# Kernel optimization log

Hardware: AMD Instinct MI355X
Metric: run time of the kernel (lower is better)

The kernel has to match this reference:

```python
import jax, jax.numpy as jnp
import numpy as np
import math

L, D, H, DK, DFF, B, S = 4, 512, 8, 256, 2048, 8, 256
HD = H * DK
EPS = 1e-6


def _norm(x, alpha, bias):
    # torch: alpha*(x-mean)/(std_unbiased + eps) + bias  (std uses ddof=1)
    mu = x.mean(axis=-1, keepdims=True)
    var = ((x - mu) ** 2).sum(axis=-1, keepdims=True) / (x.shape[-1] - 1)
    return alpha * (x - mu) / (jnp.sqrt(var) + EPS) + bias


def _positional_encoding():
    pos = jnp.arange(S, dtype=jnp.float32)[:, None]          # [S,1]
    i = jnp.arange(0, D, 2, dtype=jnp.float32)               # even indices
    pe_sin = jnp.sin(pos / (S ** (2.0 * i / D)))             # [S,D/2]
    pe_cos = jnp.cos(pos / (S ** (2.0 * (i + 1.0) / D)))     # [S,D/2]
    pe = jnp.zeros((S, D), dtype=jnp.float32)
    pe = pe.at[:, 0::2].set(pe_sin).at[:, 1::2].set(pe_cos)
    return pe


def setup_inputs() -> dict:
    key = jax.random.key(0)
    ks = jax.random.split(key, 16)
    sc = 0.02
    inp = {
        "data": jax.random.normal(ks[0], (B, S, D), dtype=jnp.float32),
        "attn_m": jax.random.randint(ks[1], (B, S), 0, 2, dtype=jnp.int32),
        "view_idx": 0,
        "seg_emb": jax.random.normal(ks[2], (3, D), dtype=jnp.float32) * sc,
        "Wq": jax.random.normal(ks[3], (L, D, HD), dtype=jnp.float32) * sc,
        "bq": jnp.zeros((L, HD), dtype=jnp.float32),
        "Wk": jax.random.normal(ks[4], (L, D, HD), dtype=jnp.float32) * sc,
        "bk": jnp.zeros((L, HD), dtype=jnp.float32),
        "Wv": jax.random.normal(ks[5], (L, D, HD), dtype=jnp.float32) * sc,
        "bv": jnp.zeros((L, HD), dtype=jnp.float32),
        "Wo": jax.random.normal(ks[6], (L, HD, D), dtype=jnp.float32) * sc,
        "bo": jnp.zeros((L, D), dtype=jnp.float32),
        "W1": jax.random.normal(ks[7], (L, D, DFF), dtype=jnp.float32) * sc,
        "b1": jnp.zeros((L, DFF), dtype=jnp.float32),
        "W2": jax.random.normal(ks[8], (L, DFF, D), dtype=jnp.float32) * sc,
        "b2": jnp.zeros((L, D), dtype=jnp.float32),
        "alpha1": jnp.ones((L, D), dtype=jnp.float32),
        "bias1": jnp.zeros((L, D), dtype=jnp.float32),
        "alpha2": jnp.ones((L, D), dtype=jnp.float32),
        "bias2": jnp.zeros((L, D), dtype=jnp.float32),
        "alpha_f": jnp.ones((D,), dtype=jnp.float32),
        "bias_f": jnp.zeros((D,), dtype=jnp.float32),
    }
    return inp


def reference(data, attn_m, view_idx, seg_emb, Wq, bq, Wk, bk, Wv, bv, Wo, bo,
              W1, b1, W2, b2, alpha1, bias1, alpha2, bias2, alpha_f, bias_f):
    # positional encoder: x*sqrt(d_f) + pe + seg_embedding(view_idx*seq_len)
    pe = _positional_encoding()
    seg_idx = view_idx * S  # scalar; must be < 3 (view_idx == 0 in practice)
    x = data * math.sqrt(D) + pe[None, :, :] + seg_emb[seg_idx][None, None, :]

    # mask: attn_m [B,S] -> [B,1,1,S] bool, True = masked (key axis)
    maskb = attn_m.astype(bool)[:, None, None, :]

    for i in range(L):
        x2 = _norm(x, alpha1[i], bias1[i])
        q = (x2 @ Wq[i] + bq[i]).reshape(B, S, H, DK).transpose(0, 2, 1, 3)
        k = (x2 @ Wk[i] + bk[i]).reshape(B, S, H, DK).transpose(0, 2, 1, 3)
        v = (x2 @ Wv[i] + bv[i]).reshape(B, S, H, DK).transpose(0, 2, 1, 3)
        scores = jnp.einsum('bhqd,bhkd->bhqk', q, k) / math.sqrt(DK)
        scores = jnp.where(maskb, -1e9, scores)
        attnw = jax.nn.softmax(scores, axis=-1)
        o = jnp.einsum('bhqk,bhkd->bhqd', attnw, v)
        o = o.transpose(0, 2, 1, 3).reshape(B, S, HD) @ Wo[i] + bo[i]
        x = x + o
        x2 = _norm(x, alpha2[i], bias2[i])
        ff = jax.nn.relu(x2 @ W1[i] + b1[i]) @ W2[i] + b2[i]
        x = x + ff

    return _norm(x, alpha_f, bias_f)
```

## Files before the change

### kernel.cpp

```cpp
#include <hip/hip_runtime.h>
#include <hip/hip_bf16.h>

#define LNUM 4
#define DIM  512
#define SS   256

typedef unsigned short ushort_t;
typedef __attribute__((ext_vector_type(8))) short bf16x8;
typedef __attribute__((ext_vector_type(4))) float f32x4;
typedef __attribute__((ext_vector_type(8))) unsigned short u16x8;

#define VWAIT(n) asm volatile("s_waitcnt vmcnt(" #n ")" ::: "memory")
__device__ __forceinline__ void bar() { __builtin_amdgcn_s_barrier(); }

__device__ __forceinline__ ushort_t f2b(float f) {
  union { float f; unsigned u; } x; x.f = f;
  unsigned r = x.u + 0x7FFFu + ((x.u >> 16) & 1u);
  return (ushort_t)(r >> 16);
}

__device__ __forceinline__ void gload16(const void* g, void* s) {
  __builtin_amdgcn_global_load_lds((const __attribute__((address_space(1))) void*)g,
                                   (__attribute__((address_space(3))) void*)s, 16, 0, 0);
}

template<int TM, int TN, int EPI, int NBUF>
__global__ __launch_bounds__(256, 2)
void gemm_bt(const ushort_t* __restrict__ A, const ushort_t* __restrict__ B,
             const float* __restrict__ bias, const float* __restrict__ bias2,
             const float* __restrict__ bias3,
             ushort_t* __restrict__ outB, ushort_t* __restrict__ outB2,
             ushort_t* __restrict__ outB3, float* __restrict__ outF,
             int K, int lda, int ldb, int ldc, int nkz, int relu,
             long zA, long zB)
{
  constexpr int CA = TM / 32, CB = TN / 32, SN = CA + CB;
  constexpr int WM = TM / 32, WN = TN / 32;
  constexpr bool BATCH = (EPI == 4);
  __shared__ ushort_t As[NBUF * TM * 64];
  __shared__ ushort_t Bs[NBUF * TN * 64];
  const int tid = threadIdx.x, lane = tid & 63, wid = tid >> 6;
  const int wm = wid >> 1, wn = wid & 1;
  const int z = blockIdx.z;
  const int kz = BATCH ? 0 : z;
  const int Kz = K / nkz, k0 = kz * Kz, nt = Kz >> 6;

  const ushort_t* Ab = A + (BATCH ? (long)z * zA : 0) + (long)blockIdx.y * TM * lda + k0;
  const ushort_t* Bb = B + (BATCH ? (long)z * zB : 0) + (long)blockIdx.x * TN * ldb + k0;

  const ushort_t* srcA[CA]; ushort_t* ldsA[CA];
  const ushort_t* srcB[CB]; ushort_t* ldsB[CB];
#pragma unroll
  for (int c = 0; c < CA; ++c) {
    int off = c * 4096 + tid * 16;
    int row = off >> 7;
    int scol = ((off & 127) ^ ((row & 7) << 4)) >> 1;
    srcA[c] = Ab + (long)row * lda + scol;
    ldsA[c] = As + c * 2048 + wid * 512;
  }
#pragma unroll
  for (int c = 0; c < CB; ++c) {
    int off = c * 4096 + tid * 16;
    int row = off >> 7;
    int scol = ((off & 127) ^ ((row & 7) << 4)) >> 1;
    srcB[c] = Bb + (long)row * ldb + scol;
    ldsB[c] = Bs + c * 2048 + wid * 512;
  }

  f32x4 acc[WM][WN] = {};

  auto STAGE = [&](int buf, int t) {
#pragma unroll
    for (int c = 0; c < CA; ++c) gload16(srcA[c] + t * 64, ldsA[c] + buf * TM * 64);
#pragma unroll
    for (int c = 0; c < CB; ++c) gload16(srcB[c] + t * 64, ldsB[c] + buf * TN * 64);
  };

  auto COMPUTE = [&](int buf) {
#pragma unroll
    for (int ks = 0; ks < 2; ++ks) {
      const int kb = ks * 64 + ((lane >> 4) << 4);
      bf16x8 af[WM], bfr[WN];
#pragma unroll
      for (int f = 0; f < WM; ++f) {
        int ra = wm * (TM / 2) + f * 16 + (lane & 15);
        af[f] = *(const bf16x8*)((const char*)As + buf * TM * 128 + ra * 128 + (kb ^ ((ra & 7) << 4)));
      }
#pragma unroll
      for (int g = 0; g < WN; ++g) {
        int rb = wn * (TN / 2) + g * 16 + (lane & 15);
        bfr[g] = *(const bf16x8*)((const char*)Bs + buf * TN * 128 + rb * 128 + (kb ^ ((rb & 7) << 4)));
      }
      __builtin_amdgcn_s_setprio(1);
#pragma unroll
      for (int i = 0; i < WM; ++i)
#pragma unroll
        for (int j = 0; j < WN; ++j)
          acc[i][j] = __builtin_amdgcn_mfma_f32_16x16x32_bf16(af[i], bfr[j], acc[i][j], 0, 0, 0);
      __builtin_amdgcn_s_setprio(0);
    }
  };

  STAGE(0, 0);
  if constexpr (NBUF == 3) {
    STAGE(1, 1);
    for (int t = 0; t < nt; ++t) {
      if (t < nt - 1) { if constexpr (SN == 6) VWAIT(6); else VWAIT(4); }
      else VWAIT(0);
      bar();
      if (t + 2 < nt) STAGE((t + 2) % 3, t + 2);
      COMPUTE(t % 3);
    }
  } else {
    for (int t = 0; t < nt; ++t) {
      VWAIT(0);
      bar();
      if (t + 1 < nt) STAGE((t + 1) & 1, t + 1);
      COMPUTE(t & 1);
    }
  }

  const int row0 = blockIdx.y * TM + wm * (TM / 2) + ((lane >> 4) << 2);
  int col0 = blockIdx.x * TN + wn * (TN / 2) + (lane & 15);
  const float* bsel = bias;
  ushort_t* osel = outB;
  int seg = 0;
  if (EPI == 3) {
    seg = (blockIdx.x * TN) >> 11;
    if (seg == 1) { bsel = bias2; osel = outB2; }
    else if (seg == 2) { bsel = bias3; }
    col0 -= seg * 2048;
  }

  if (EPI == 3 && seg == 2) {
    ushort_t* Vt = As;
    const int colvBase = blockIdx.x * TN - 4096;
    const int rowBase = blockIdx.y * TM;
    const int h = colvBase >> 8, dk0 = colvBase & 255;
    const int bh = ((rowBase >> 8) << 3) + h;
    const int s0 = rowBase & 255;
    bar();
    if constexpr (TN == 64) {
#pragma unroll
      for (int i = 0; i < WM; ++i)
#pragma unroll
        for (int j = 0; j < WN; ++j) {
          const int colL = wn * (TN / 2) + j * 16 + (lane & 15);
          const float bv = bsel[col0 + j * 16];
#pragma unroll
          for (int r = 0; r < 4; ++r) {
            const int rowL = wm * (TM / 2) + i * 16 + ((lane >> 4) << 2) + r;
            Vt[colL * 136 + rowL] = f2b(acc[i][j][r] + bv);
          }
        }
      bar();
      const int dkl = tid >> 2, scc = (tid & 3) * 32;
      ushort_t* dst = outB3 + ((long)bh << 16) + (long)(dk0 + dkl) * 256 + s0 + scc;
#pragma unroll
      for (int m = 0; m < 4; ++m)
        *(u16x8*)(dst + m * 8) = *(const u16x8*)(Vt + dkl * 136 + scc + m * 8);
    } else {
#pragma unroll
      for (int half = 0; half < 2; ++half) {
        if (half) bar();
        if (wn == half) {
#pragma unroll
          for (int i = 0; i < WM; ++i)
#pragma unroll
            for (int j = 0; j < WN; ++j) {
              const int colL = j * 16 + (lane & 15);
              const float bv = bsel[col0 + j * 16];
#pragma unroll
              for (int r = 0; r < 4; ++r) {
                const int rowL = wm * 64 + i * 16 + ((lane >> 4) << 2) + r;
                Vt[colL * 136 + rowL] = f2b(acc[i][j][r] + bv);
              }
            }
        }
        bar();
        const int dkl = tid >> 2, scc = (tid & 3) * 32;
        ushort_t* dst = outB3 + ((long)bh << 16) +
                        (long)(dk0 + half * 64 + dkl) * 256 + s0 + scc;
#pragma unroll
        for (int m = 0; m < 4; ++m)
          *(u16x8*)(dst + m * 8) = *(const u16x8*)(Vt + dkl * 136 + scc + m * 8);
      }
    }
    return;
  }

#pragma unroll
  for (int i = 0; i < WM; ++i) {
#pragma unroll
    for (int j = 0; j < WN; ++j) {
      const int col = col0 + j * 16;
      float bv = 0.f;
      if (EPI == 2) bv = (kz == 0) ? bias[col] : 0.f;
      else if (EPI == 0 || EPI == 3) bv = bsel[col];
#pragma unroll
      for (int r = 0; r < 4; ++r) {
        const int row = row0 + i * 16 + r;
        float v = acc[i][j][r] + bv;
        if (EPI == 2) {
          outF[(long)kz * 1048576 + (long)row * ldc + col] = v;
        } else if (EPI == 3) {
          const long addr = (((long)(row >> 8) * 8 + (col >> 8)) << 16) +
                            (long)(row & 255) * 256 + (col & 255);
          osel[addr] = f2b(v);
        } else if (EPI == 4) {
          const int bb = z >> 3, hh = z & 7;
          osel[(long)(bb * 256 + row) * 2048 + hh * 256 + col] = f2b(acc[i][j][r]);
        } else {
          if (relu) v = fmaxf(v, 0.f);
          osel[(long)row * ldc + col] = f2b(v);
        }
      }
    }
  }
}

__global__ __launch_bounds__(256, 2)
void scoresm_k(const ushort_t* __restrict__ qh, const ushort_t* __restrict__ kh,
               const int* __restrict__ attnm, ushort_t* __restrict__ P)
{
  __shared__ ushort_t As[2][64 * 64];
  __shared__ ushort_t Bs[2][256 * 64];
  const int bh = blockIdx.x, qt = blockIdx.y;
  const int b = bh >> 3;
  const int tid = threadIdx.x, lane = tid & 63, wid = tid >> 6;
  const int l15 = lane & 15, l4 = lane >> 4;

  unsigned mbits = 0;
#pragma unroll
  for (int j = 0; j < 16; ++j)
    mbits |= (attnm[b * 256 + j * 16 + l15] != 0 ? 1u : 0u) << j;

  const ushort_t* Qb = qh + ((long)bh << 16) + qt * 64 * 256;
  const ushort_t* Kb = kh + ((long)bh << 16);
  const ushort_t* srcA[2]; ushort_t* ldsA[2];
  const ushort_t* srcB[8]; ushort_t* ldsB[8];
#pragma unroll
  for (int c = 0; c < 2; ++c) {
    int off = c * 4096 + tid * 16;
    int row = off >> 7;
    int scol = ((off & 127) ^ ((row & 7) << 4)) >> 1;
    srcA[c] = Qb + (long)row * 256 + scol;
    ldsA[c] = As[0] + c * 2048 + wid * 512;
  }
#pragma unroll
  for (int c = 0; c < 8; ++c) {
    int off = c * 4096 + tid * 16;
    int row = off >> 7;
    int scol = ((off & 127) ^ ((row & 7) << 4)) >> 1;
    srcB[c] = Kb + (long)row * 256 + scol;
    ldsB[c] = Bs[0] + c * 2048 + wid * 512;
  }

  auto STAGE = [&](int buf, int t) {
#pragma unroll
    for (int c = 0; c < 2; ++c) gload16(srcA[c] + t * 64, ldsA[c] + buf * 4096);
#pragma unroll
    for (int c = 0; c < 8; ++c) gload16(srcB[c] + t * 64, ldsB[c] + buf * 16384);
  };

  f32x4 sacc[16] = {};
  STAGE(0, 0);
  for (int t = 0; t < 4; ++t) {
    VWAIT(0);
    bar();
    if (t < 3) STAGE((t + 1) & 1, t + 1);
    const int buf = t & 1;
#pragma unroll
    for (int ks = 0; ks < 2; ++ks) {
      const int kb = ks * 64 + (l4 << 4);
      const int ra = wid * 16 + l15;
      bf16x8 af = *(const bf16x8*)((const char*)As[buf] + ra * 128 + (kb ^ ((ra & 7) << 4)));
      __builtin_amdgcn_s_setprio(1);
#pragma unroll
      for (int j = 0; j < 16; ++j) {
        const int rb = j * 16 + l15;
        bf16x8 bf_ = *(const bf16x8*)((const char*)Bs[buf] + rb * 128 + (kb ^ ((rb & 7) << 4)));
        sacc[j] = __builtin_amdgcn_mfma_f32_16x16x32_bf16(af, bf_, sacc[j], 0, 0, 0);
      }
      __builtin_amdgcn_s_setprio(0);
    }
  }

  float mr[4] = {-3e38f, -3e38f, -3e38f, -3e38f}, sr[4] = {};
#pragma unroll
  for (int j = 0; j < 16; ++j) {
    const bool mk = (mbits >> j) & 1;
#pragma unroll
    for (int r = 0; r < 4; ++r) {
      float s = mk ? -1e9f : sacc[j][r] * 0.0625f;
      sacc[j][r] = s;
      mr[r] = fmaxf(mr[r], s);
    }
  }
#pragma unroll
  for (int o = 1; o < 16; o <<= 1)
#pragma unroll
    for (int r = 0; r < 4; ++r) mr[r] = fmaxf(mr[r], __shfl_xor(mr[r], o, 16));
#pragma unroll
  for (int j = 0; j < 16; ++j)
#pragma unroll
    for (int r = 0; r < 4; ++r) {
      float e = __expf(sacc[j][r] - mr[r]);
      sacc[j][r] = e;
      sr[r] += e;
    }
#pragma unroll
  for (int o = 1; o < 16; o <<= 1)
#pragma unroll
    for (int r = 0; r < 4; ++r) sr[r] += __shfl_xor(sr[r], o, 16);
#pragma unroll
  for (int r = 0; r < 4; ++r) sr[r] = 1.f / sr[r];

  ushort_t* Rp = (ushort_t*)Bs;
  bar();
#pragma unroll
  for (int j = 0; j < 16; ++j)
#pragma unroll
    for (int r = 0; r < 4; ++r) {
      const int row = wid * 16 + l4 * 4 + r;
      *(ushort_t*)((char*)Rp + row * 512 + (((j * 16 + l15) * 2) ^ ((row & 7) << 4))) =
          f2b(sacc[j][r] * sr[r]);
    }
  bar();
  const int row = tid >> 2, cb0 = (tid & 3) * 128;
  ushort_t* dst = P + ((long)bh << 16) + (long)(qt * 64 + row) * 256 + (cb0 >> 1);
#pragma unroll
  for (int m = 0; m < 8; ++m) {
    u16x8 v = *(const u16x8*)((const char*)Rp + row * 512 + ((cb0 + m * 16) ^ ((row & 7) << 4)));
    *(u16x8*)(dst + m * 8) = v;
  }
}

__global__ __launch_bounds__(256)
void build_x(const float* __restrict__ data, const float* __restrict__ seg,
             const int* __restrict__ viewp, float* __restrict__ x)
{
  int i = blockIdx.x * 256 + threadIdx.x;
  int d = i & 511;
  int s = (i >> 9) & 255;
  float ang = (float)s * exp2f((float)d * -0.03125f);
  float pe = (d & 1) ? cosf(ang) : sinf(ang);
  int vrow = viewp[0] * SS;
  x[i] = data[i] * 22.627416997969522f + pe + seg[vrow * DIM + d];
}

__global__ __launch_bounds__(256)
void lnorm_k(const float* __restrict__ x, const float* __restrict__ parts, int np,
             float* __restrict__ xout,
             const float* __restrict__ alpha, const float* __restrict__ beta,
             ushort_t* __restrict__ outB, float* __restrict__ outF)
{
  const int row = blockIdx.x, tid = threadIdx.x;
  const long base = (long)row * DIM;
  float2 v = ((const float2*)(x + base))[tid];
  if (np) {
    for (int p = 0; p < np; ++p) {
      float2 a = ((const float2*)(parts + (long)p * 1048576 + base))[tid];
      v.x += a.x; v.y += a.y;
    }
    ((float2*)(xout + base))[tid] = v;
  }
  float s = v.x + v.y;
#pragma unroll
  for (int o = 32; o; o >>= 1) s += __shfl_xor(s, o, 64);
  __shared__ float rs[4], rq[4];
  if ((tid & 63) == 0) rs[tid >> 6] = s;
  __syncthreads();
  const float mu = (rs[0] + rs[1] + rs[2] + rs[3]) * (1.f / 512.f);
  const float dx = v.x - mu, dy = v.y - mu;
  float q = dx * dx + dy * dy;
#pragma unroll
  for (int o = 32; o; o >>= 1) q += __shfl_xor(q, o, 64);
  if ((tid & 63) == 0) rq[tid >> 6] = q;
  __syncthreads();
  const float var = (rq[0] + rq[1] + rq[2] + rq[3]) * (1.f / 511.f);
  const float rstd = 1.f / (sqrtf(var) + 1e-6f);
  const int d0 = tid * 2;
  const float o0 = alpha[d0] * dx * rstd + beta[d0];
  const float o1 = alpha[d0 + 1] * dy * rstd + beta[d0 + 1];
  if (outB) { outB[base + d0] = f2b(o0); outB[base + d0 + 1] = f2b(o1); }
  else      { outF[base + d0] = o0;      outF[base + d0 + 1] = o1; }
}

__global__ __launch_bounds__(256)
void wtransA(const float* __restrict__ Wq, const float* __restrict__ Wk,
             const float* __restrict__ Wv, const float* __restrict__ W1,
             ushort_t* __restrict__ qkvW, ushort_t* __restrict__ W1T)
{
  __shared__ float t[32][33];
  const int z = blockIdx.z, widx = z >> 2, layer = z & 3;
  const float* src = (widx == 0) ? Wq : (widx == 1) ? Wk : (widx == 2) ? Wv : W1;
  src += (long)layer * 512 * 2048;
  ushort_t* dst = (widx == 3) ? (W1T + (long)layer * 2048 * 512)
                              : (qkvW + (long)layer * (6144L * 512) + (long)widx * 2048 * 512);
  const int c0 = blockIdx.x * 32, r0 = blockIdx.y * 32;
  const int tx = threadIdx.x & 31, ty = threadIdx.x >> 5;
#pragma unroll
  for (int i = 0; i < 4; ++i) t[ty + i * 8][tx] = src[(long)(r0 + ty + i * 8) * 2048 + c0 + tx];
  __syncthreads();
#pragma unroll
  for (int i = 0; i < 4; ++i) dst[(long)(c0 + ty + i * 8) * 512 + r0 + tx] = f2b(t[tx][ty + i * 8]);
}

__global__ __launch_bounds__(256)
void wtransB(const float* __restrict__ Wo, const float* __restrict__ W2,
             ushort_t* __restrict__ WoT, ushort_t* __restrict__ W2T)
{
  __shared__ float t[32][33];
  const int z = blockIdx.z, widx = z >> 2, layer = z & 3;
  const float* src = ((widx == 0) ? Wo : W2) + (long)layer * 2048 * 512;
  ushort_t* dst = ((widx == 0) ? WoT : W2T) + (long)layer * 512 * 2048;
  const int c0 = blockIdx.x * 32, r0 = blockIdx.y * 32;
  const int tx = threadIdx.x & 31, ty = threadIdx.x >> 5;
#pragma unroll
  for (int i = 0; i < 4; ++i) t[ty + i * 8][tx] = src[(long)(r0 + ty + i * 8) * 512 + c0 + tx];
  __syncthreads();
#pragma unroll
  for (int i = 0; i < 4; ++i) dst[(long)(c0 + ty + i * 8) * 2048 + r0 + tx] = f2b(t[tx][ty + i * 8]);
}

extern "C" void kernel_launch(void* const* d_in, const int* in_sizes, int n_in,
                              void* d_out, int out_size, void* d_ws, size_t ws_size,
                              hipStream_t stream)
{
  const float* data  = (const float*)d_in[0];
  const int*   attnm = (const int*)d_in[1];
  const int*   viewp = (const int*)d_in[2];
  const float* seg   = (const float*)d_in[3];
  const float* Wq    = (const float*)d_in[4];
  const float* bq    = (const float*)d_in[5];
  const float* Wk    = (const float*)d_in[6];
  const float* bk    = (const float*)d_in[7];
  const float* Wv    = (const float*)d_in[8];
  const float* bv    = (const float*)d_in[9];
  const float* Wo    = (const float*)d_in[10];
  const float* bo    = (const float*)d_in[11];
  const float* W1    = (const float*)d_in[12];
  const float* b1    = (const float*)d_in[13];
  const float* W2    = (const float*)d_in[14];
  const float* b2    = (const float*)d_in[15];
  const float* al1   = (const float*)d_in[16];
  const float* be1   = (const float*)d_in[17];
  const float* al2   = (const float*)d_in[18];
  const float* be2   = (const float*)d_in[19];
  const float* alf   = (const float*)d_in[20];
  const float* bef   = (const float*)d_in[21];

  char* w = (char*)d_ws;
  const size_t MB = 1024 * 1024;
  ushort_t* qkvW = (ushort_t*)(w + 0 * MB);
  ushort_t* WoT  = (ushort_t*)(w + 24 * MB);
  ushort_t* W1T  = (ushort_t*)(w + 32 * MB);
  ushort_t* W2T  = (ushort_t*)(w + 40 * MB);
  float*    x    = (float*)   (w + 48 * MB);
  ushort_t* x2   = (ushort_t*)(w + 52 * MB);
  ushort_t* qb   = (ushort_t*)(w + 54 * MB);
  ushort_t* kbf  = (ushort_t*)(w + 62 * MB);
  ushort_t* vT   = (ushort_t*)(w + 70 * MB);
  ushort_t* ao   = (ushort_t*)(w + 78 * MB);
  ushort_t* ffh  = (ushort_t*)(w + 86 * MB);
  float*    parts= (float*)   (w + 94 * MB);
  ushort_t* P    = (ushort_t*)(w + 110 * MB);

  dim3 blk(256);
  const long QKV_L = 6144L * 512;
  wtransA<<<dim3(64, 16, 16), blk, 0, stream>>>(Wq, Wk, Wv, W1, qkvW, W1T);
  wtransB<<<dim3(16, 64, 8), blk, 0, stream>>>(Wo, W2, WoT, W2T);
  build_x<<<4096, blk, 0, stream>>>(data, seg, viewp, x);

  for (int i = 0; i < LNUM; ++i) {
    if (i == 0)
      lnorm_k<<<2048, blk, 0, stream>>>(x, nullptr, 0, nullptr, al1, be1, x2, nullptr);
    gemm_bt<128, 128, 3, 2><<<dim3(48, 16, 1), blk, 0, stream>>>(
        x2, qkvW + (long)i * QKV_L, bq + i * 2048, bk + i * 2048, bv + i * 2048,
        qb, kbf, vT, nullptr, 512, 512, 512, 2048, 1, 0, 0, 0);
    scoresm_k<<<dim3(64, 4), blk, 0, stream>>>(qb, kbf, attnm, P);
    gemm_bt<128, 64, 4, 3><<<dim3(4, 2, 64), blk, 0, stream>>>(
        P, vT, nullptr, nullptr, nullptr,
        ao, nullptr, nullptr, nullptr, 256, 256, 256, 2048, 1, 0,
        65536, 65536);
    gemm_bt<64, 64, 2, 3><<<dim3(8, 32, 2), blk, 0, stream>>>(
        ao, WoT + (long)i * 512 * 2048, bo + i * 512, nullptr, nullptr,
        nullptr, nullptr, nullptr, parts, 2048, 2048, 2048, 512, 2, 0, 0, 0);
    lnorm_k<<<2048, blk, 0, stream>>>(x, parts, 2, x, al2 + i * 512, be2 + i * 512, x2, nullptr);
    gemm_bt<128, 64, 0, 3><<<dim3(32, 16, 1), blk, 0, stream>>>(
        x2, W1T + (long)i * 2048 * 512, b1 + i * 2048, nullptr, nullptr,
        ffh, nullptr, nullptr, nullptr, 512, 512, 512, 2048, 1, 1, 0, 0);
    gemm_bt<64, 64, 2, 3><<<dim3(8, 32, 2), blk, 0, stream>>>(
        ffh, W2T + (long)i * 512 * 2048, b2 + i * 512, nullptr, nullptr,
        nullptr, nullptr, nullptr, parts, 2048, 2048, 2048, 512, 2, 0, 0, 0);
    if (i < LNUM - 1)
      lnorm_k<<<2048, blk, 0, stream>>>(x, parts, 2, x, al1 + (i + 1) * 512, be1 + (i + 1) * 512, x2, nullptr);
    else
      lnorm_k<<<2048, blk, 0, stream>>>(x, parts, 2, x, alf, bef, nullptr, (float*)d_out);
  }
}
```

Baseline: 431.4 us.

## Fuse attention P·V product into the scores/softmax kernel

The softmax kernel now keeps the normalized probability tile in LDS and loads it into registers. It then streams V^T chunks through double-buffered LDS to compute P·V with MFMA, writing the head output directly into the concatenated layout. This removes the separate batched GEMM launch and the global round trip of the probability matrix P. In exchange, the attention work runs on only 256 blocks with more serial work each, which may leave much of the GPU idle.

```diff
diff --git a/kernel.cpp b/kernel.cpp
--- a/kernel.cpp
+++ b/kernel.cpp
@@ -31,22 +31,19 @@
              const float* __restrict__ bias3,
              ushort_t* __restrict__ outB, ushort_t* __restrict__ outB2,
              ushort_t* __restrict__ outB3, float* __restrict__ outF,
-             int K, int lda, int ldb, int ldc, int nkz, int relu,
-             long zA, long zB)
+             int K, int lda, int ldb, int ldc, int nkz, int relu)
 {
   constexpr int CA = TM / 32, CB = TN / 32, SN = CA + CB;
   constexpr int WM = TM / 32, WN = TN / 32;
-  constexpr bool BATCH = (EPI == 4);
   __shared__ ushort_t As[NBUF * TM * 64];
   __shared__ ushort_t Bs[NBUF * TN * 64];
   const int tid = threadIdx.x, lane = tid & 63, wid = tid >> 6;
   const int wm = wid >> 1, wn = wid & 1;
-  const int z = blockIdx.z;
-  const int kz = BATCH ? 0 : z;
+  const int kz = blockIdx.z;
   const int Kz = K / nkz, k0 = kz * Kz, nt = Kz >> 6;
 
-  const ushort_t* Ab = A + (BATCH ? (long)z * zA : 0) + (long)blockIdx.y * TM * lda + k0;
-  const ushort_t* Bb = B + (BATCH ? (long)z * zB : 0) + (long)blockIdx.x * TN * ldb + k0;
+  const ushort_t* Ab = A + (long)blockIdx.y * TM * lda + k0;
+  const ushort_t* Bb = B + (long)blockIdx.x * TN * ldb + k0;
 
   const ushort_t* srcA[CA]; ushort_t* ldsA[CA];
   const ushort_t* srcB[CB]; ushort_t* ldsB[CB];
@@ -140,51 +137,30 @@
     const int bh = ((rowBase >> 8) << 3) + h;
     const int s0 = rowBase & 255;
     bar();
-    if constexpr (TN == 64) {
-#pragma unroll
-      for (int i = 0; i < WM; ++i)
-#pragma unroll
-        for (int j = 0; j < WN; ++j) {
-          const int colL = wn * (TN / 2) + j * 16 + (lane & 15);
-          const float bv = bsel[col0 + j * 16];
-#pragma unroll
-          for (int r = 0; r < 4; ++r) {
-            const int rowL = wm * (TM / 2) + i * 16 + ((lane >> 4) << 2) + r;
-            Vt[colL * 136 + rowL] = f2b(acc[i][j][r] + bv);
+#pragma unroll
+    for (int half = 0; half < 2; ++half) {
+      if (half) bar();
+      if (wn == half) {
+#pragma unroll
+        for (int i = 0; i < WM; ++i)
+#pragma unroll
+          for (int j = 0; j < WN; ++j) {
+            const int colL = j * 16 + (lane & 15);
+            const float bv = bsel[col0 + j * 16];
+#pragma unroll
+            for (int r = 0; r < 4; ++r) {
+              const int rowL = wm * 64 + i * 16 + ((lane >> 4) << 2) + r;
+              Vt[colL * 136 + rowL] = f2b(acc[i][j][r] + bv);
+            }
           }
-        }
+      }
       bar();
       const int dkl = tid >> 2, scc = (tid & 3) * 32;
-      ushort_t* dst = outB3 + ((long)bh << 16) + (long)(dk0 + dkl) * 256 + s0 + scc;
+      ushort_t* dst = outB3 + ((long)bh << 16) +
+                      (long)(dk0 + half * 64 + dkl) * 256 + s0 + scc;
 #pragma unroll
       for (int m = 0; m < 4; ++m)
         *(u16x8*)(dst + m * 8) = *(const u16x8*)(Vt + dkl * 136 + scc + m * 8);
-    } else {
-#pragma unroll
-      for (int half = 0; half < 2; ++half) {
-        if (half) bar();
-        if (wn == half) {
-#pragma unroll
-          for (int i = 0; i < WM; ++i)
-#pragma unroll
-            for (int j = 0; j < WN; ++j) {
-              const int colL = j * 16 + (lane & 15);
-              const float bv = bsel[col0 + j * 16];
-#pragma unroll
-              for (int r = 0; r < 4; ++r) {
-                const int rowL = wm * 64 + i * 16 + ((lane >> 4) << 2) + r;
-                Vt[colL * 136 + rowL] = f2b(acc[i][j][r] + bv);
-              }
-            }
-        }
-        bar();
-        const int dkl = tid >> 2, scc = (tid & 3) * 32;
-        ushort_t* dst = outB3 + ((long)bh << 16) +
-                        (long)(dk0 + half * 64 + dkl) * 256 + s0 + scc;
-#pragma unroll
-        for (int m = 0; m < 4; ++m)
-          *(u16x8*)(dst + m * 8) = *(const u16x8*)(Vt + dkl * 136 + scc + m * 8);
-      }
     }
     return;
   }
@@ -207,9 +183,6 @@
           const long addr = (((long)(row >> 8) * 8 + (col >> 8)) << 16) +
                             (long)(row & 255) * 256 + (col & 255);
           osel[addr] = f2b(v);
-        } else if (EPI == 4) {
-          const int bb = z >> 3, hh = z & 7;
-          osel[(long)(bb * 256 + row) * 2048 + hh * 256 + col] = f2b(acc[i][j][r]);
         } else {
           if (relu) v = fmaxf(v, 0.f);
           osel[(long)row * ldc + col] = f2b(v);
@@ -220,13 +193,14 @@
 }
 
 __global__ __launch_bounds__(256, 2)
-void scoresm_k(const ushort_t* __restrict__ qh, const ushort_t* __restrict__ kh,
-               const int* __restrict__ attnm, ushort_t* __restrict__ P)
+void attnf_k(const ushort_t* __restrict__ qh, const ushort_t* __restrict__ kh,
+             const ushort_t* __restrict__ vT, const int* __restrict__ attnm,
+             ushort_t* __restrict__ ao)
 {
   __shared__ ushort_t As[2][64 * 64];
   __shared__ ushort_t Bs[2][256 * 64];
   const int bh = blockIdx.x, qt = blockIdx.y;
-  const int b = bh >> 3;
+  const int b = bh >> 3, h = bh & 7;
   const int tid = threadIdx.x, lane = tid & 63, wid = tid >> 6;
   const int l15 = lane & 15, l4 = lane >> 4;
 
@@ -326,14 +300,62 @@
       *(ushort_t*)((char*)Rp + row * 512 + (((j * 16 + l15) * 2) ^ ((row & 7) << 4))) =
           f2b(sacc[j][r] * sr[r]);
     }
+  bf16x8 pf[8];
+  {
+    const int ra = wid * 16 + l15;
+#pragma unroll
+    for (int ks = 0; ks < 8; ++ks)
+      pf[ks] = *(const bf16x8*)((const char*)Rp + ra * 512 +
+                                ((ks * 64 + (l4 << 4)) ^ ((ra & 7) << 4)));
+  }
   bar();
-  const int row = tid >> 2, cb0 = (tid & 3) * 128;
-  ushort_t* dst = P + ((long)bh << 16) + (long)(qt * 64 + row) * 256 + (cb0 >> 1);
-#pragma unroll
-  for (int m = 0; m < 8; ++m) {
-    u16x8 v = *(const u16x8*)((const char*)Rp + row * 512 + ((cb0 + m * 16) ^ ((row & 7) << 4)));
-    *(u16x8*)(dst + m * 8) = v;
-  }
+
+  const ushort_t* Vb = vT + ((long)bh << 16);
+  int velem[8];
+#pragma unroll
+  for (int c = 0; c < 8; ++c) {
+    int off = c * 4096 + tid * 16;
+    int row = off >> 9;
+    int colb = (off & 511) ^ ((row & 7) << 4);
+    velem[c] = row * 256 + (colb >> 1);
+  }
+  auto VSTAGE = [&](int buf, int ch) {
+#pragma unroll
+    for (int c = 0; c < 8; ++c)
+      gload16(Vb + (long)ch * 16384 + velem[c], Bs[buf] + c * 2048 + wid * 512);
+  };
+
+  f32x4 oacc[16] = {};
+  VSTAGE(0, 0);
+  for (int ch = 0; ch < 4; ++ch) {
+    VWAIT(0);
+    bar();
+    if (ch < 3) VSTAGE((ch + 1) & 1, ch + 1);
+    const char* vb = (const char*)Bs[ch & 1];
+#pragma unroll
+    for (int ks = 0; ks < 8; ++ks) {
+      const int kb = ks * 64 + (l4 << 4);
+      __builtin_amdgcn_s_setprio(1);
+#pragma unroll
+      for (int j = 0; j < 4; ++j) {
+        const int rb = j * 16 + l15;
+        bf16x8 vf = *(const bf16x8*)(vb + rb * 512 + (kb ^ ((rb & 7) << 4)));
+        oacc[ch * 4 + j] = __builtin_amdgcn_mfma_f32_16x16x32_bf16(pf[ks], vf, oacc[ch * 4 + j], 0, 0, 0);
+      }
+      __builtin_amdgcn_s_setprio(0);
+    }
+  }
+
+  const int rowq = qt * 64 + wid * 16 + (l4 << 2);
+#pragma unroll
+  for (int ch = 0; ch < 4; ++ch)
+#pragma unroll
+    for (int j = 0; j < 4; ++j) {
+      const int dk = ch * 64 + j * 16 + l15;
+#pragma unroll
+      for (int r = 0; r < 4; ++r)
+        ao[(long)(b * 256 + rowq + r) * 2048 + h * 256 + dk] = f2b(oacc[ch * 4 + j][r]);
+    }
 }
 
 __global__ __launch_bounds__(256)
@@ -465,7 +487,6 @@
   ushort_t* ao   = (ushort_t*)(w + 78 * MB);
   ushort_t* ffh  = (ushort_t*)(w + 86 * MB);
   float*    parts= (float*)   (w + 94 * MB);
-  ushort_t* P    = (ushort_t*)(w + 110 * MB);
 
   dim3 blk(256);
   const long QKV_L = 6144L * 512;
@@ -478,22 +499,18 @@
       lnorm_k<<<2048, blk, 0, stream>>>(x, nullptr, 0, nullptr, al1, be1, x2, nullptr);
     gemm_bt<128, 128, 3, 2><<<dim3(48, 16, 1), blk, 0, stream>>>(
         x2, qkvW + (long)i * QKV_L, bq + i * 2048, bk + i * 2048, bv + i * 2048,
-        qb, kbf, vT, nullptr, 512, 512, 512, 2048, 1, 0, 0, 0);
-    scoresm_k<<<dim3(64, 4), blk, 0, stream>>>(qb, kbf, attnm, P);
-    gemm_bt<128, 64, 4, 3><<<dim3(4, 2, 64), blk, 0, stream>>>(
-        P, vT, nullptr, nullptr, nullptr,
-        ao, nullptr, nullptr, nullptr, 256, 256, 256, 2048, 1, 0,
-        65536, 65536);
+        qb, kbf, vT, nullptr, 512, 512, 512, 2048, 1, 0);
+    attnf_k<<<dim3(64, 4), blk, 0, stream>>>(qb, kbf, vT, attnm, ao);
     gemm_bt<64, 64, 2, 3><<<dim3(8, 32, 2), blk, 0, stream>>>(
         ao, WoT + (long)i * 512 * 2048, bo + i * 512, nullptr, nullptr,
-        nullptr, nullptr, nullptr, parts, 2048, 2048, 2048, 512, 2, 0, 0, 0);
+        nullptr, nullptr, nullptr, parts, 2048, 2048, 2048, 512, 2, 0);
     lnorm_k<<<2048, blk, 0, stream>>>(x, parts, 2, x, al2 + i * 512, be2 + i * 512, x2, nullptr);
     gemm_bt<128, 64, 0, 3><<<dim3(32, 16, 1), blk, 0, stream>>>(
         x2, W1T + (long)i * 2048 * 512, b1 + i * 2048, nullptr, nullptr,
-        ffh, nullptr, nullptr, nullptr, 512, 512, 512, 2048, 1, 1, 0, 0);
+        ffh, nullptr, nullptr, nullptr, 512, 512, 512, 2048, 1, 1);
     gemm_bt<64, 64, 2, 3><<<dim3(8, 32, 2), blk, 0, stream>>>(
         ffh, W2T + (long)i * 512 * 2048, b2 + i * 512, nullptr, nullptr,
-        nullptr, nullptr, nullptr, parts, 2048, 2048, 2048, 512, 2, 0, 0, 0);
+        nullptr, nullptr, nullptr, parts, 2048, 2048, 2048, 512, 2, 0);
     if (i < LNUM - 1)
       lnorm_k<<<2048, blk, 0, stream>>>(x, parts, 2, x, al1 + (i + 1) * 512, be1 + (i + 1) * 512, x2, nullptr);
     else
```

New measurement: 401.3 us. 1.08x faster.
